# Kernel tuning notes

Hardware: AMD Instinct MI355X
Metric: run time of the kernel (lower is better)

## Reference

```python
import jax, jax.numpy as jnp
import numpy as np

D_MODEL = 1024
D_STATE = 16
D_CONV = 4
EXPAND = 2
D_INNER = EXPAND * D_MODEL
DT_RANK = (D_MODEL + 15) // 16  # ceil(d_model/16) = 64


def setup_inputs() -> dict:
    key = jax.random.key(0)
    ks = jax.random.split(key, 12)
    B, L = 2, 2048
    s = lambda k, shape, sc: jax.random.normal(k, shape, dtype=jnp.float32) * sc
    inp = {
        "x": s(ks[0], (B, L, D_MODEL), 1.0),
        "in_proj_w": s(ks[1], (2 * D_INNER, D_MODEL), 0.02),
        "conv_w": s(ks[2], (D_INNER, 1, D_CONV), 0.2),
        "conv_b": s(ks[3], (D_INNER,), 0.02),
        "x_proj_w": s(ks[4], (DT_RANK + 2 * D_STATE, D_INNER), 0.02),
        "dt_proj_w": s(ks[5], (D_INNER, DT_RANK), 0.05),
        "dt_proj_b": s(ks[6], (D_INNER,), 0.5),
        # A_log init: log(1..d_state) per channel (standard S4D-real init)
        "A_log": jnp.broadcast_to(jnp.log(jnp.arange(1, D_STATE + 1, dtype=jnp.float32)), (D_INNER, D_STATE)).copy(),
        "D": jnp.ones((D_INNER,), dtype=jnp.float32),
        "out_proj_w": s(ks[7], (D_MODEL, D_INNER), 0.02),
        "ln_g": jnp.ones((D_MODEL,), dtype=jnp.float32),
        "ln_b": jnp.zeros((D_MODEL,), dtype=jnp.float32),
    }
    return inp


def _mamba(x, in_proj_w, conv_w, conv_b, x_proj_w, dt_proj_w, dt_proj_b, A_log, D, out_proj_w):
    Bsz, L, _ = x.shape
    # input projection -> x branch and gate z
    xz = jnp.einsum("bld,ed->ble", x, in_proj_w)  # [B, L, 2*d_inner]
    xi, z = jnp.split(xz, 2, axis=-1)
    # causal depthwise conv over time
    xc = jnp.swapaxes(xi, 1, 2)  # [B, d_inner, L]
    xc = jax.lax.conv_general_dilated(
        xc, conv_w, window_strides=(1,), padding=[(D_CONV - 1, 0)],
        feature_group_count=D_INNER, dimension_numbers=("NCH", "OIH", "NCH"))
    xc = xc + conv_b[None, :, None]
    xc = jnp.swapaxes(xc, 1, 2)  # [B, L, d_inner]
    xc = jax.nn.silu(xc)
    # data-dependent dt, B, C
    x_dbl = jnp.einsum("bld,ed->ble", xc, x_proj_w)
    dt_r = x_dbl[..., :DT_RANK]
    Bm = x_dbl[..., DT_RANK:DT_RANK + D_STATE]      # [B, L, d_state]
    Cm = x_dbl[..., DT_RANK + D_STATE:]             # [B, L, d_state]
    dt = jax.nn.softplus(jnp.einsum("blr,er->ble", dt_r, dt_proj_w) + dt_proj_b)  # [B, L, d_inner]
    A = -jnp.exp(A_log)  # [d_inner, d_state]

    # selective scan: h_t = exp(dt_t*A) h_{t-1} + dt_t*B_t*u_t ; y_t = C_t . h_t
    def step(h, inps):
        dt_t, B_t, C_t, u_t = inps  # [B,d_inner],[B,d_state],[B,d_state],[B,d_inner]
        dA = jnp.exp(dt_t[..., None] * A)                       # [B, d_inner, d_state]
        dBu = (dt_t * u_t)[..., None] * B_t[:, None, :]          # [B, d_inner, d_state]
        h = dA * h + dBu
        y = jnp.einsum("bds,bs->bd", h, C_t)
        return h, y

    h0 = jnp.zeros((Bsz, D_INNER, D_STATE), dtype=x.dtype)
    xs = (jnp.swapaxes(dt, 0, 1), jnp.swapaxes(Bm, 0, 1), jnp.swapaxes(Cm, 0, 1), jnp.swapaxes(xc, 0, 1))
    _, ys = jax.lax.scan(step, h0, xs)
    y = jnp.swapaxes(ys, 0, 1) + D * xc  # skip term
    y = y * jax.nn.silu(z)
    return jnp.einsum("ble,de->bld", y, out_proj_w)


def _layernorm(x, g, b, eps=1e-5):
    mu = jnp.mean(x, axis=-1, keepdims=True)
    var = jnp.mean(jnp.square(x - mu), axis=-1, keepdims=True)
    return (x - mu) * jax.lax.rsqrt(var + eps) * g + b


def reference(x, in_proj_w, conv_w, conv_b, x_proj_w, dt_proj_w, dt_proj_b, A_log, D, out_proj_w, ln_g, ln_b):
    y = _mamba(x, in_proj_w, conv_w, conv_b, x_proj_w, dt_proj_w, dt_proj_b, A_log, D, out_proj_w)
    return _layernorm(y + x, ln_g, ln_b)
```

## Files before the change

kernel.cpp:

```cpp
#include <hip/hip_runtime.h>
#include <math.h>

#define D_STATE 16
#define D_INNER 2048
#define SEQ     2048
#define BSZ     2
#define NTOK    (BSZ*SEQ)
#define CH      32
#define NCHK    (SEQ/CH)
#define HLOFF   ((size_t)2048 * 4096)

typedef __bf16 bf16x8 __attribute__((ext_vector_type(8)));
typedef float  floatx4 __attribute__((ext_vector_type(4)));

__device__ __forceinline__ unsigned short f2bf(float f) {
  unsigned int u = __float_as_uint(f);
  u += 0x7fff + ((u >> 16) & 1);
  return (unsigned short)(u >> 16);
}

__device__ __forceinline__ void gload16(const unsigned short* g, unsigned short* l) {
  __builtin_amdgcn_global_load_lds(
      (const __attribute__((address_space(1))) unsigned int*)g,
      (__attribute__((address_space(3))) unsigned int*)l, 16, 0, 0);
}

__global__ __launch_bounds__(256) void cast_k(
    const float* __restrict__ src, unsigned short* __restrict__ dst, int n)
{
  int i = (blockIdx.x * 256 + threadIdx.x) * 4;
  if (i < n) {
    float4 v = *(const float4*)(src + i);
    ushort4 o;
    o.x = f2bf(v.x); o.y = f2bf(v.y); o.z = f2bf(v.z); o.w = f2bf(v.w);
    *(ushort4*)(dst + i) = o;
  }
}

__global__ __launch_bounds__(256) void cast_dtr(
    const float* __restrict__ src, unsigned short* __restrict__ dst)
{
  int i = (blockIdx.x * 256 + threadIdx.x) * 4;
  int m = i >> 6, col = i & 63;
  float4 v = *(const float4*)(src + (size_t)m * 96 + col);
  ushort4 o;
  o.x = f2bf(v.x); o.y = f2bf(v.y); o.z = f2bf(v.z); o.w = f2bf(v.w);
  *(ushort4*)(dst + (size_t)m * 64 + col) = o;
}

template<int MODE>
__global__ __launch_bounds__(256) void mgemm(
    const unsigned short* __restrict__ A, int lda,
    const unsigned short* __restrict__ W, int ldw,
    float* __restrict__ C, int ldc,
    int N, int ksl, const float* __restrict__ aux, size_t slicesz)
{
  __shared__ unsigned short As[128 * 32];
  __shared__ unsigned short Ws[128 * 32];
  const int tid  = threadIdx.x;
  const int wave = tid >> 6, lane = tid & 63;
  const int m0 = blockIdx.y * 128, n0 = blockIdx.x * 128;
  const int k0 = blockIdx.z * ksl;
  C += (size_t)blockIdx.z * slicesz;
  const int srow = lane >> 2;
  const int scol = ((((lane & 3) + 4) - ((lane >> 3) & 3)) & 3) * 8;
  const int fr = lane & 15, fq = lane >> 4;
  const int sw = (fr >> 1) & 3;
  const int wm = (wave >> 1) * 64, wn = (wave & 1) * 64;

  const int ar0 = (wave * 2 + 0) * 16 + srow;
  const int ar1 = (wave * 2 + 1) * 16 + srow;
  int wr0 = n0 + ar0; if (wr0 > N - 1) wr0 = N - 1;
  int wr1 = n0 + ar1; if (wr1 > N - 1) wr1 = N - 1;
  const unsigned short* gA0 = A + (size_t)(m0 + ar0) * lda + scol;
  const unsigned short* gA1 = A + (size_t)(m0 + ar1) * lda + scol;
  const unsigned short* gW0 = W + (size_t)wr0 * ldw + scol;
  const unsigned short* gW1 = W + (size_t)wr1 * ldw + scol;
  unsigned short* lA0 = As + (wave * 2 + 0) * 512;
  unsigned short* lA1 = As + (wave * 2 + 1) * 512;
  unsigned short* lW0 = Ws + (wave * 2 + 0) * 512;
  unsigned short* lW1 = Ws + (wave * 2 + 1) * 512;

  floatx4 zero = {0.f, 0.f, 0.f, 0.f};
  floatx4 acc[4][4];
#pragma unroll
  for (int i = 0; i < 4; ++i)
#pragma unroll
    for (int j = 0; j < 4; ++j) acc[i][j] = zero;

  for (int kt = k0; kt < k0 + ksl; kt += 32) {
    __syncthreads();
    gload16(gA0 + kt, lA0);
    gload16(gA1 + kt, lA1);
    gload16(gW0 + kt, lW0);
    gload16(gW1 + kt, lW1);
    __syncthreads();
    bf16x8 af[4], bfr[4];
#pragma unroll
    for (int i = 0; i < 4; ++i) {
      int cuA = ((fq + sw) & 3) * 8;
      af[i]  = *(const bf16x8*)(As + (wm + i * 16 + fr) * 32 + cuA);
      bfr[i] = *(const bf16x8*)(Ws + (wn + i * 16 + fr) * 32 + cuA);
    }
#pragma unroll
    for (int i = 0; i < 4; ++i)
#pragma unroll
      for (int j = 0; j < 4; ++j)
        acc[i][j] = __builtin_amdgcn_mfma_f32_16x16x32_bf16(af[i], bfr[j], acc[i][j], 0, 0, 0);
  }

#pragma unroll
  for (int i = 0; i < 4; ++i) {
#pragma unroll
    for (int j = 0; j < 4; ++j) {
      int n = n0 + wn + j * 16 + fr;
      if (n < N) {
#pragma unroll
        for (int r = 0; r < 4; ++r) {
          int m = m0 + wm + i * 16 + fq * 4 + r;
          float v = acc[i][j][r];
          if (MODE == 1) { v += aux[n]; v = (v > 20.f) ? v : log1pf(__expf(v)); }
          if (MODE == 2) v += aux[(size_t)m * ldc + n];
          C[(size_t)m * ldc + n] = v;
        }
      }
    }
  }
}

__global__ __launch_bounds__(256) void reduce_96(
    const float* __restrict__ p, float* __restrict__ dst)
{
  int i = (blockIdx.x * 256 + threadIdx.x) * 4;
  float4 s = *(const float4*)(p + i);
#pragma unroll
  for (int z = 1; z < 8; ++z) {
    float4 v = *(const float4*)(p + (size_t)z * (4096 * 96) + i);
    s.x += v.x; s.y += v.y; s.z += v.z; s.w += v.w;
  }
  *(float4*)(dst + i) = s;
}

__global__ __launch_bounds__(256) void conv_silu_k(
    const float* __restrict__ xz, const float* __restrict__ w,
    const float* __restrict__ b, float* __restrict__ xc,
    unsigned short* __restrict__ xcb)
{
  int idx = blockIdx.x * 256 + threadIdx.x;
  int e  = idx & (D_INNER - 1);
  int bl = idx >> 11;
  int l  = bl & (SEQ - 1);
  float acc = b[e];
#pragma unroll
  for (int k = 0; k < 4; ++k) {
    int ll = l - 3 + k;
    if (ll >= 0)
      acc = fmaf(xz[(size_t)(bl + ll - l) * 4096 + e], w[e * 4 + k], acc);
  }
  float v = acc / (1.f + __expf(-acc));
  xc[idx] = v;
  xcb[idx] = f2bf(v);
}

__global__ __launch_bounds__(256) void scan_p1(
    const float* __restrict__ A_log,
    const float* __restrict__ x_dbl, const float* __restrict__ xc,
    const float* __restrict__ dt, float* __restrict__ xz)
{
  const int t = blockIdx.x * 256 + threadIdx.x;
  const int d = t & 2047;
  const int c = (t >> 11) & (NCHK - 1);
  const int b = t >> 17;
  const size_t tok0 = (size_t)b * SEQ + c * CH;
  const float* xd = x_dbl + tok0 * 96;

  float Ac[16];
  {
    float4 a0 = *(const float4*)(A_log + d * 16);
    float4 a1 = *(const float4*)(A_log + d * 16 + 4);
    float4 a2 = *(const float4*)(A_log + d * 16 + 8);
    float4 a3 = *(const float4*)(A_log + d * 16 + 12);
    Ac[0]=-__expf(a0.x); Ac[1]=-__expf(a0.y); Ac[2]=-__expf(a0.z); Ac[3]=-__expf(a0.w);
    Ac[4]=-__expf(a1.x); Ac[5]=-__expf(a1.y); Ac[6]=-__expf(a1.z); Ac[7]=-__expf(a1.w);
    Ac[8]=-__expf(a2.x); Ac[9]=-__expf(a2.y); Ac[10]=-__expf(a2.z); Ac[11]=-__expf(a2.w);
    Ac[12]=-__expf(a3.x); Ac[13]=-__expf(a3.y); Ac[14]=-__expf(a3.z); Ac[15]=-__expf(a3.w);
  }

  float p[16], h[16];
#pragma unroll
  for (int s = 0; s < 16; ++s) { p[s] = 1.f; h[s] = 0.f; }

  for (int l = 0; l < CH; ++l) {
    float dtv = dt[(tok0 + l) * 2048 + d];
    float uv  = xc[(tok0 + l) * 2048 + d];
    float du  = dtv * uv;
    float Bv[16];
#pragma unroll
    for (int j = 0; j < 4; ++j) {
      float4 bb = *(const float4*)(xd + l * 96 + 64 + j * 4);
      Bv[j*4+0]=bb.x; Bv[j*4+1]=bb.y; Bv[j*4+2]=bb.z; Bv[j*4+3]=bb.w;
    }
#pragma unroll
    for (int s = 0; s < 16; ++s) {
      float dA = __expf(dtv * Ac[s]);
      p[s] *= dA;
      h[s] = fmaf(dA, h[s], du * Bv[s]);
    }
  }

  float* pp = xz + ((size_t)(t >> 7)) * 4096 + ((t << 4) & 2047);
#pragma unroll
  for (int j = 0; j < 4; ++j) {
    *(float4*)(pp + j * 4)         = make_float4(p[j*4], p[j*4+1], p[j*4+2], p[j*4+3]);
    *(float4*)(pp + HLOFF + j * 4) = make_float4(h[j*4], h[j*4+1], h[j*4+2], h[j*4+3]);
  }
}

__global__ __launch_bounds__(256) void scan_fix(float* __restrict__ xz)
{
  int tid = blockIdx.x * 256 + threadIdx.x;
  int s = tid & 15;
  int d = (tid >> 4) & 2047;
  int b = tid >> 15;
  float h = 0.f;
  for (int c = 0; c < NCHK; ++c) {
    size_t idx = ((((size_t)(b * NCHK + c) * 2048) + d) * 16) + s;
    size_t addr = (idx >> 11) * 4096 + (idx & 2047);
    float p  = xz[addr];
    float hl = xz[addr + HLOFF];
    xz[addr + HLOFF] = h;
    h = fmaf(p, h, hl);
  }
}

__global__ __launch_bounds__(256) void scan_p2(
    const float* __restrict__ A_log, const float* __restrict__ Dvec,
    const float* __restrict__ x_dbl, const float* __restrict__ xc,
    const float* __restrict__ xz, const float* __restrict__ dt,
    unsigned short* __restrict__ ybf)
{
  const int t = blockIdx.x * 256 + threadIdx.x;
  const int d = t & 2047;
  const int c = (t >> 11) & (NCHK - 1);
  const int b = t >> 17;
  const size_t tok0 = (size_t)b * SEQ + c * CH;
  const float* xd = x_dbl + tok0 * 96;
  const float Dd = Dvec[d];

  float Ac[16];
  {
    float4 a0 = *(const float4*)(A_log + d * 16);
    float4 a1 = *(const float4*)(A_log + d * 16 + 4);
    float4 a2 = *(const float4*)(A_log + d * 16 + 8);
    float4 a3 = *(const float4*)(A_log + d * 16 + 12);
    Ac[0]=-__expf(a0.x); Ac[1]=-__expf(a0.y); Ac[2]=-__expf(a0.z); Ac[3]=-__expf(a0.w);
    Ac[4]=-__expf(a1.x); Ac[5]=-__expf(a1.y); Ac[6]=-__expf(a1.z); Ac[7]=-__expf(a1.w);
    Ac[8]=-__expf(a2.x); Ac[9]=-__expf(a2.y); Ac[10]=-__expf(a2.z); Ac[11]=-__expf(a2.w);
    Ac[12]=-__expf(a3.x); Ac[13]=-__expf(a3.y); Ac[14]=-__expf(a3.z); Ac[15]=-__expf(a3.w);
  }

  const float* pp = xz + ((size_t)(t >> 7)) * 4096 + ((t << 4) & 2047);
  float h[16];
#pragma unroll
  for (int j = 0; j < 4; ++j) {
    float4 hh = *(const float4*)(pp + HLOFF + j * 4);
    h[j*4+0]=hh.x; h[j*4+1]=hh.y; h[j*4+2]=hh.z; h[j*4+3]=hh.w;
  }

  for (int l = 0; l < CH; ++l) {
    float dtv = dt[(tok0 + l) * 2048 + d];
    float uv  = xc[(tok0 + l) * 2048 + d];
    float zv  = xz[(tok0 + l) * 4096 + 2048 + d];
    float du  = dtv * uv;
    float Bv[16], Cv[16];
#pragma unroll
    for (int j = 0; j < 4; ++j) {
      float4 bb = *(const float4*)(xd + l * 96 + 64 + j * 4);
      float4 cc = *(const float4*)(xd + l * 96 + 80 + j * 4);
      Bv[j*4+0]=bb.x; Bv[j*4+1]=bb.y; Bv[j*4+2]=bb.z; Bv[j*4+3]=bb.w;
      Cv[j*4+0]=cc.x; Cv[j*4+1]=cc.y; Cv[j*4+2]=cc.z; Cv[j*4+3]=cc.w;
    }
    float y = 0.f;
#pragma unroll
    for (int s = 0; s < 16; ++s) {
      float dA = __expf(dtv * Ac[s]);
      h[s] = fmaf(dA, h[s], du * Bv[s]);
      y = fmaf(h[s], Cv[s], y);
    }
    y = fmaf(Dd, uv, y);
    y *= zv / (1.f + __expf(-zv));
    ybf[(tok0 + l) * 2048 + d] = f2bf(y);
  }
}

__global__ __launch_bounds__(256) void ln2_k(
    const float* __restrict__ p0, const float* __restrict__ p1,
    const float* __restrict__ x, const float* __restrict__ g,
    const float* __restrict__ bb, float* __restrict__ out)
{
  int row = blockIdx.x;
  size_t off = (size_t)row * 1024;
  float4 a = ((const float4*)(p0 + off))[threadIdx.x];
  float4 b = ((const float4*)(p1 + off))[threadIdx.x];
  float4 c = ((const float4*)(x  + off))[threadIdx.x];
  float4 v;
  v.x = a.x + b.x + c.x; v.y = a.y + b.y + c.y;
  v.z = a.z + b.z + c.z; v.w = a.w + b.w + c.w;
  float s  = v.x + v.y + v.z + v.w;
  float sq = v.x * v.x + v.y * v.y + v.z * v.z + v.w * v.w;
#pragma unroll
  for (int o = 32; o >= 1; o >>= 1) {
    s  += __shfl_xor(s,  o, 64);
    sq += __shfl_xor(sq, o, 64);
  }
  __shared__ float red[8];
  int wid = threadIdx.x >> 6;
  if ((threadIdx.x & 63) == 0) { red[wid] = s; red[4 + wid] = sq; }
  __syncthreads();
  s  = red[0] + red[1] + red[2] + red[3];
  sq = red[4] + red[5] + red[6] + red[7];
  float mu  = s * (1.f / 1024.f);
  float var = sq * (1.f / 1024.f) - mu * mu;
  float r   = rsqrtf(var + 1e-5f);
  int col = threadIdx.x * 4;
  float4 gv = *(const float4*)(g + col);
  float4 bv = *(const float4*)(bb + col);
  float4 o;
  o.x = (v.x - mu) * r * gv.x + bv.x;
  o.y = (v.y - mu) * r * gv.y + bv.y;
  o.z = (v.z - mu) * r * gv.z + bv.z;
  o.w = (v.w - mu) * r * gv.w + bv.w;
  ((float4*)(out + off))[threadIdx.x] = o;
}

extern "C" void kernel_launch(void* const* d_in, const int* in_sizes, int n_in,
                              void* d_out, int out_size, void* d_ws, size_t ws_size,
                              hipStream_t stream)
{
  const float* x       = (const float*)d_in[0];
  const float* in_proj = (const float*)d_in[1];
  const float* conv_w  = (const float*)d_in[2];
  const float* conv_b  = (const float*)d_in[3];
  const float* x_proj  = (const float*)d_in[4];
  const float* dt_w    = (const float*)d_in[5];
  const float* dt_b    = (const float*)d_in[6];
  const float* A_log   = (const float*)d_in[7];
  const float* Dv      = (const float*)d_in[8];
  const float* out_w   = (const float*)d_in[9];
  const float* ln_g    = (const float*)d_in[10];
  const float* ln_bias = (const float*)d_in[11];
  float* out = (float*)d_out;

  float* ws   = (float*)d_ws;
  float* xz   = ws;
  float* xc   = xz   + (size_t)NTOK * 4096;
  float* xdbl = xc   + (size_t)NTOK * 2048;
  float* dty  = xdbl + (size_t)NTOK * 96;
  unsigned short* xc_bf = (unsigned short*)(dty + (size_t)NTOK * 2048);
  unsigned short* y_bf  = xc_bf + (size_t)NTOK * 2048;
  unsigned short* wbuf  = y_bf  + (size_t)NTOK * 2048;
  unsigned short* x_bf  = (unsigned short*)dty;
  unsigned short* dtr_bf = xc_bf;
  float* pbufx = dty;
  float* pbufo = xz;

  dim3 blk(256);
  cast_k<<<dim3(NTOK * 1024 / 1024), blk, 0, stream>>>(x, x_bf, NTOK * 1024);
  cast_k<<<dim3(4096 * 1024 / 1024), blk, 0, stream>>>(in_proj, wbuf, 4096 * 1024);
  mgemm<0><<<dim3(32, 32, 1), blk, 0, stream>>>(x_bf, 1024, wbuf, 1024,
                                                xz, 4096, 4096, 1024, nullptr, 0);
  conv_silu_k<<<dim3((NTOK * D_INNER) / 256), blk, 0, stream>>>(xz, conv_w, conv_b, xc, xc_bf);
  cast_k<<<dim3(96 * 2048 / 1024), blk, 0, stream>>>(x_proj, wbuf, 96 * 2048);
  mgemm<0><<<dim3(1, 32, 8), blk, 0, stream>>>(xc_bf, 2048, wbuf, 2048,
                                               pbufx, 96, 96, 256, nullptr,
                                               (size_t)4096 * 96);
  reduce_96<<<dim3(4096 * 96 / 1024), blk, 0, stream>>>(pbufx, xdbl);
  cast_dtr<<<dim3(NTOK * 64 / 1024), blk, 0, stream>>>(xdbl, dtr_bf);
  cast_k<<<dim3(2048 * 64 / 1024), blk, 0, stream>>>(dt_w, wbuf, 2048 * 64);
  mgemm<1><<<dim3(16, 32, 1), blk, 0, stream>>>(dtr_bf, 64, wbuf, 64,
                                                dty, 2048, 2048, 64, dt_b, 0);
  scan_p1 <<<dim3(BSZ * NCHK * 2048 / 256), blk, 0, stream>>>(A_log, xdbl, xc, dty, xz);
  scan_fix<<<dim3(BSZ * 2048 * 16 / 256), blk, 0, stream>>>(xz);
  scan_p2 <<<dim3(BSZ * NCHK * 2048 / 256), blk, 0, stream>>>(A_log, Dv, xdbl, xc, xz, dty, y_bf);
  cast_k<<<dim3(1024 * 2048 / 1024), blk, 0, stream>>>(out_w, wbuf, 1024 * 2048);
  mgemm<0><<<dim3(8, 32, 2), blk, 0, stream>>>(y_bf, 2048, wbuf, 2048,
                                               pbufo, 1024, 1024, 1024, nullptr,
                                               (size_t)4096 * 1024);
  ln2_k<<<dim3(NTOK), blk, 0, stream>>>(pbufo, pbufo + (size_t)4096 * 1024,
                                        x, ln_g, ln_bias, out);
}
```

Baseline: 393.1 us.

## Store xz and xc intermediates in bf16, fuse casts and reduce kernels

The in_proj GEMM now writes xz directly as bf16, and the conv kernel reads bf16, processes 4 channels per thread and writes only a bf16 xc. The scan kernels read the bf16 xc and z. The chunk prefix state moves to its own contiguous buffer. The two input casts are merged into one kernel, and the x_proj split-K reduce is fused with the dt_r bf16 cast. This cuts memory traffic and launch count, at the cost of lower precision for the scan input u and the gate z.

```diff
diff --git a/kernel.cpp b/kernel.cpp
--- a/kernel.cpp
+++ b/kernel.cpp
@@ -8,7 +8,7 @@
 #define NTOK    (BSZ*SEQ)
 #define CH      32
 #define NCHK    (SEQ/CH)
-#define HLOFF   ((size_t)2048 * 4096)
+#define PHN     ((size_t)BSZ * NCHK * 2048 * 16)
 
 typedef __bf16 bf16x8 __attribute__((ext_vector_type(8)));
 typedef float  floatx4 __attribute__((ext_vector_type(4)));
@@ -17,6 +17,9 @@
   unsigned int u = __float_as_uint(f);
   u += 0x7fff + ((u >> 16) & 1);
   return (unsigned short)(u >> 16);
+}
+__device__ __forceinline__ float bf2f(unsigned short u) {
+  return __uint_as_float((unsigned int)u << 16);
 }
 
 __device__ __forceinline__ void gload16(const unsigned short* g, unsigned short* l) {
@@ -37,22 +40,46 @@
   }
 }
 
-__global__ __launch_bounds__(256) void cast_dtr(
-    const float* __restrict__ src, unsigned short* __restrict__ dst)
+__global__ __launch_bounds__(256) void cast2_k(
+    const float* __restrict__ s1, unsigned short* __restrict__ d1, int n1,
+    const float* __restrict__ s2, unsigned short* __restrict__ d2, int n2)
 {
   int i = (blockIdx.x * 256 + threadIdx.x) * 4;
-  int m = i >> 6, col = i & 63;
-  float4 v = *(const float4*)(src + (size_t)m * 96 + col);
+  const float* s; unsigned short* d;
+  if (i < n1) { s = s1 + i; d = d1 + i; }
+  else if (i < n1 + n2) { s = s2 + (i - n1); d = d2 + (i - n1); }
+  else return;
+  float4 v = *(const float4*)s;
   ushort4 o;
   o.x = f2bf(v.x); o.y = f2bf(v.y); o.z = f2bf(v.z); o.w = f2bf(v.w);
-  *(ushort4*)(dst + (size_t)m * 64 + col) = o;
+  *(ushort4*)d = o;
+}
+
+__global__ __launch_bounds__(256) void redcast_k(
+    const float* __restrict__ p, float* __restrict__ dst,
+    unsigned short* __restrict__ dtr)
+{
+  int i = (blockIdx.x * 256 + threadIdx.x) * 4;
+  float4 s = *(const float4*)(p + i);
+#pragma unroll
+  for (int z = 1; z < 8; ++z) {
+    float4 v = *(const float4*)(p + (size_t)z * (4096 * 96) + i);
+    s.x += v.x; s.y += v.y; s.z += v.z; s.w += v.w;
+  }
+  *(float4*)(dst + i) = s;
+  int m = i / 96, col = i - m * 96;
+  if (col < 64) {
+    ushort4 o;
+    o.x = f2bf(s.x); o.y = f2bf(s.y); o.z = f2bf(s.z); o.w = f2bf(s.w);
+    *(ushort4*)(dtr + (size_t)m * 64 + col) = o;
+  }
 }
 
 template<int MODE>
 __global__ __launch_bounds__(256) void mgemm(
     const unsigned short* __restrict__ A, int lda,
     const unsigned short* __restrict__ W, int ldw,
-    float* __restrict__ C, int ldc,
+    void* __restrict__ Cv_, int ldc,
     int N, int ksl, const float* __restrict__ aux, size_t slicesz)
 {
   __shared__ unsigned short As[128 * 32];
@@ -61,7 +88,6 @@
   const int wave = tid >> 6, lane = tid & 63;
   const int m0 = blockIdx.y * 128, n0 = blockIdx.x * 128;
   const int k0 = blockIdx.z * ksl;
-  C += (size_t)blockIdx.z * slicesz;
   const int srow = lane >> 2;
   const int scol = ((((lane & 3) + 4) - ((lane >> 3) & 3)) & 3) * 8;
   const int fr = lane & 15, fq = lane >> 4;
@@ -120,52 +146,58 @@
           int m = m0 + wm + i * 16 + fq * 4 + r;
           float v = acc[i][j][r];
           if (MODE == 1) { v += aux[n]; v = (v > 20.f) ? v : log1pf(__expf(v)); }
-          if (MODE == 2) v += aux[(size_t)m * ldc + n];
-          C[(size_t)m * ldc + n] = v;
+          if (MODE == 3) {
+            ((unsigned short*)Cv_)[(size_t)m * ldc + n] = f2bf(v);
+          } else {
+            float* C = (float*)Cv_ + (size_t)blockIdx.z * slicesz;
+            C[(size_t)m * ldc + n] = v;
+          }
         }
       }
     }
   }
 }
 
-__global__ __launch_bounds__(256) void reduce_96(
-    const float* __restrict__ p, float* __restrict__ dst)
-{
-  int i = (blockIdx.x * 256 + threadIdx.x) * 4;
-  float4 s = *(const float4*)(p + i);
-#pragma unroll
-  for (int z = 1; z < 8; ++z) {
-    float4 v = *(const float4*)(p + (size_t)z * (4096 * 96) + i);
-    s.x += v.x; s.y += v.y; s.z += v.z; s.w += v.w;
-  }
-  *(float4*)(dst + i) = s;
-}
-
 __global__ __launch_bounds__(256) void conv_silu_k(
-    const float* __restrict__ xz, const float* __restrict__ w,
-    const float* __restrict__ b, float* __restrict__ xc,
-    unsigned short* __restrict__ xcb)
-{
-  int idx = blockIdx.x * 256 + threadIdx.x;
-  int e  = idx & (D_INNER - 1);
-  int bl = idx >> 11;
+    const unsigned short* __restrict__ xzb, const float* __restrict__ w,
+    const float* __restrict__ b, unsigned short* __restrict__ xcb)
+{
+  int gid = blockIdx.x * 256 + threadIdx.x;
+  int e4 = (gid * 4) & 2047;
+  int bl = gid >> 9;
   int l  = bl & (SEQ - 1);
-  float acc = b[e];
+  float4 acc = *(const float4*)(b + e4);
+  float4 w0 = *(const float4*)(w + (e4 + 0) * 4);
+  float4 w1 = *(const float4*)(w + (e4 + 1) * 4);
+  float4 w2 = *(const float4*)(w + (e4 + 2) * 4);
+  float4 w3 = *(const float4*)(w + (e4 + 3) * 4);
+  const float* w0p = (const float*)&w0;
+  const float* w1p = (const float*)&w1;
+  const float* w2p = (const float*)&w2;
+  const float* w3p = (const float*)&w3;
 #pragma unroll
   for (int k = 0; k < 4; ++k) {
     int ll = l - 3 + k;
-    if (ll >= 0)
-      acc = fmaf(xz[(size_t)(bl + ll - l) * 4096 + e], w[e * 4 + k], acc);
-  }
-  float v = acc / (1.f + __expf(-acc));
-  xc[idx] = v;
-  xcb[idx] = f2bf(v);
+    if (ll >= 0) {
+      ushort4 xv = *(const ushort4*)(xzb + (size_t)(bl - 3 + k) * 4096 + e4);
+      acc.x = fmaf(bf2f(xv.x), w0p[k], acc.x);
+      acc.y = fmaf(bf2f(xv.y), w1p[k], acc.y);
+      acc.z = fmaf(bf2f(xv.z), w2p[k], acc.z);
+      acc.w = fmaf(bf2f(xv.w), w3p[k], acc.w);
+    }
+  }
+  ushort4 o;
+  o.x = f2bf(acc.x / (1.f + __expf(-acc.x)));
+  o.y = f2bf(acc.y / (1.f + __expf(-acc.y)));
+  o.z = f2bf(acc.z / (1.f + __expf(-acc.z)));
+  o.w = f2bf(acc.w / (1.f + __expf(-acc.w)));
+  *(ushort4*)(xcb + (size_t)gid * 4) = o;
 }
 
 __global__ __launch_bounds__(256) void scan_p1(
     const float* __restrict__ A_log,
-    const float* __restrict__ x_dbl, const float* __restrict__ xc,
-    const float* __restrict__ dt, float* __restrict__ xz)
+    const float* __restrict__ x_dbl, const unsigned short* __restrict__ xcb,
+    const float* __restrict__ dt, float* __restrict__ PH)
 {
   const int t = blockIdx.x * 256 + threadIdx.x;
   const int d = t & 2047;
@@ -192,7 +224,7 @@
 
   for (int l = 0; l < CH; ++l) {
     float dtv = dt[(tok0 + l) * 2048 + d];
-    float uv  = xc[(tok0 + l) * 2048 + d];
+    float uv  = bf2f(xcb[(tok0 + l) * 2048 + d]);
     float du  = dtv * uv;
     float Bv[16];
 #pragma unroll
@@ -208,15 +240,15 @@
     }
   }
 
-  float* pp = xz + ((size_t)(t >> 7)) * 4096 + ((t << 4) & 2047);
+  float* pp = PH + (size_t)t * 16;
 #pragma unroll
   for (int j = 0; j < 4; ++j) {
-    *(float4*)(pp + j * 4)         = make_float4(p[j*4], p[j*4+1], p[j*4+2], p[j*4+3]);
-    *(float4*)(pp + HLOFF + j * 4) = make_float4(h[j*4], h[j*4+1], h[j*4+2], h[j*4+3]);
-  }
-}
-
-__global__ __launch_bounds__(256) void scan_fix(float* __restrict__ xz)
+    *(float4*)(pp + j * 4)       = make_float4(p[j*4], p[j*4+1], p[j*4+2], p[j*4+3]);
+    *(float4*)(pp + PHN + j * 4) = make_float4(h[j*4], h[j*4+1], h[j*4+2], h[j*4+3]);
+  }
+}
+
+__global__ __launch_bounds__(256) void scan_fix(float* __restrict__ PH)
 {
   int tid = blockIdx.x * 256 + threadIdx.x;
   int s = tid & 15;
@@ -225,19 +257,18 @@
   float h = 0.f;
   for (int c = 0; c < NCHK; ++c) {
     size_t idx = ((((size_t)(b * NCHK + c) * 2048) + d) * 16) + s;
-    size_t addr = (idx >> 11) * 4096 + (idx & 2047);
-    float p  = xz[addr];
-    float hl = xz[addr + HLOFF];
-    xz[addr + HLOFF] = h;
+    float p  = PH[idx];
+    float hl = PH[idx + PHN];
+    PH[idx + PHN] = h;
     h = fmaf(p, h, hl);
   }
 }
 
 __global__ __launch_bounds__(256) void scan_p2(
     const float* __restrict__ A_log, const float* __restrict__ Dvec,
-    const float* __restrict__ x_dbl, const float* __restrict__ xc,
-    const float* __restrict__ xz, const float* __restrict__ dt,
-    unsigned short* __restrict__ ybf)
+    const float* __restrict__ x_dbl, const unsigned short* __restrict__ xcb,
+    const unsigned short* __restrict__ xzb, const float* __restrict__ PH,
+    const float* __restrict__ dt, unsigned short* __restrict__ ybf)
 {
   const int t = blockIdx.x * 256 + threadIdx.x;
   const int d = t & 2047;
@@ -259,18 +290,18 @@
     Ac[12]=-__expf(a3.x); Ac[13]=-__expf(a3.y); Ac[14]=-__expf(a3.z); Ac[15]=-__expf(a3.w);
   }
 
-  const float* pp = xz + ((size_t)(t >> 7)) * 4096 + ((t << 4) & 2047);
+  const float* pp = PH + (size_t)t * 16;
   float h[16];
 #pragma unroll
   for (int j = 0; j < 4; ++j) {
-    float4 hh = *(const float4*)(pp + HLOFF + j * 4);
+    float4 hh = *(const float4*)(pp + PHN + j * 4);
     h[j*4+0]=hh.x; h[j*4+1]=hh.y; h[j*4+2]=hh.z; h[j*4+3]=hh.w;
   }
 
   for (int l = 0; l < CH; ++l) {
     float dtv = dt[(tok0 + l) * 2048 + d];
-    float uv  = xc[(tok0 + l) * 2048 + d];
-    float zv  = xz[(tok0 + l) * 4096 + 2048 + d];
+    float uv  = bf2f(xcb[(tok0 + l) * 2048 + d]);
+    float zv  = bf2f(xzb[(tok0 + l) * 4096 + 2048 + d]);
     float du  = dtv * uv;
     float Bv[16], Cv[16];
 #pragma unroll
@@ -351,37 +382,37 @@
   const float* ln_bias = (const float*)d_in[11];
   float* out = (float*)d_out;
 
-  float* ws   = (float*)d_ws;
-  float* xz   = ws;
-  float* xc   = xz   + (size_t)NTOK * 4096;
-  float* xdbl = xc   + (size_t)NTOK * 2048;
-  float* dty  = xdbl + (size_t)NTOK * 96;
-  unsigned short* xc_bf = (unsigned short*)(dty + (size_t)NTOK * 2048);
-  unsigned short* y_bf  = xc_bf + (size_t)NTOK * 2048;
-  unsigned short* wbuf  = y_bf  + (size_t)NTOK * 2048;
-  unsigned short* x_bf  = (unsigned short*)dty;
-  unsigned short* dtr_bf = xc_bf;
-  float* pbufx = dty;
-  float* pbufo = xz;
+  char* w8 = (char*)d_ws;
+  unsigned short* xz_bf = (unsigned short*)w8;
+  unsigned short* xc_bf = (unsigned short*)(w8 + 33554432);
+  float*          xdbl  = (float*)(w8 + 50331648);
+  float*          dty   = (float*)(w8 + 51904512);
+  unsigned short* y_bf  = (unsigned short*)(w8 + 85458944);
+  unsigned short* wbuf  = (unsigned short*)(w8 + 102236160);
+  unsigned short* x_bf  = (unsigned short*)(w8 + 110624768);
+  float*          pbufx = (float*)(w8 + 119013376);
+  float*          PH    = (float*)(w8 + 131596288);
+  float*          pbufo = (float*)xz_bf;
 
   dim3 blk(256);
-  cast_k<<<dim3(NTOK * 1024 / 1024), blk, 0, stream>>>(x, x_bf, NTOK * 1024);
-  cast_k<<<dim3(4096 * 1024 / 1024), blk, 0, stream>>>(in_proj, wbuf, 4096 * 1024);
-  mgemm<0><<<dim3(32, 32, 1), blk, 0, stream>>>(x_bf, 1024, wbuf, 1024,
-                                                xz, 4096, 4096, 1024, nullptr, 0);
-  conv_silu_k<<<dim3((NTOK * D_INNER) / 256), blk, 0, stream>>>(xz, conv_w, conv_b, xc, xc_bf);
+  cast2_k<<<dim3(2 * NTOK * 1024 / 1024), blk, 0, stream>>>(
+      x, x_bf, NTOK * 1024, in_proj, wbuf, 4096 * 1024);
+  mgemm<3><<<dim3(32, 32, 1), blk, 0, stream>>>(x_bf, 1024, wbuf, 1024,
+                                                xz_bf, 4096, 4096, 1024, nullptr, 0);
+  conv_silu_k<<<dim3((NTOK * D_INNER / 4) / 256), blk, 0, stream>>>(
+      xz_bf, conv_w, conv_b, xc_bf);
   cast_k<<<dim3(96 * 2048 / 1024), blk, 0, stream>>>(x_proj, wbuf, 96 * 2048);
   mgemm<0><<<dim3(1, 32, 8), blk, 0, stream>>>(xc_bf, 2048, wbuf, 2048,
                                                pbufx, 96, 96, 256, nullptr,
                                                (size_t)4096 * 96);
-  reduce_96<<<dim3(4096 * 96 / 1024), blk, 0, stream>>>(pbufx, xdbl);
-  cast_dtr<<<dim3(NTOK * 64 / 1024), blk, 0, stream>>>(xdbl, dtr_bf);
+  redcast_k<<<dim3(4096 * 96 / 1024), blk, 0, stream>>>(pbufx, xdbl, x_bf );
   cast_k<<<dim3(2048 * 64 / 1024), blk, 0, stream>>>(dt_w, wbuf, 2048 * 64);
-  mgemm<1><<<dim3(16, 32, 1), blk, 0, stream>>>(dtr_bf, 64, wbuf, 64,
+  mgemm<1><<<dim3(16, 32, 1), blk, 0, stream>>>(x_bf , 64, wbuf, 64,
                                                 dty, 2048, 2048, 64, dt_b, 0);
-  scan_p1 <<<dim3(BSZ * NCHK * 2048 / 256), blk, 0, stream>>>(A_log, xdbl, xc, dty, xz);
-  scan_fix<<<dim3(BSZ * 2048 * 16 / 256), blk, 0, stream>>>(xz);
-  scan_p2 <<<dim3(BSZ * NCHK * 2048 / 256), blk, 0, stream>>>(A_log, Dv, xdbl, xc, xz, dty, y_bf);
+  scan_p1 <<<dim3(BSZ * NCHK * 2048 / 256), blk, 0, stream>>>(A_log, xdbl, xc_bf, dty, PH);
+  scan_fix<<<dim3(BSZ * 2048 * 16 / 256), blk, 0, stream>>>(PH);
+  scan_p2 <<<dim3(BSZ * NCHK * 2048 / 256), blk, 0, stream>>>(A_log, Dv, xdbl, xc_bf,
+                                                              xz_bf, PH, dty, y_bf);
   cast_k<<<dim3(1024 * 2048 / 1024), blk, 0, stream>>>(out_w, wbuf, 1024 * 2048);
   mgemm<0><<<dim3(8, 32, 2), blk, 0, stream>>>(y_bf, 2048, wbuf, 2048,
                                                pbufo, 1024, 1024, 1024, nullptr,
```

New measurement: 379.1 us. 1.04x faster.
